# Kernel tuning notes

Hardware: AMD Instinct MI355X
Metric: run time of the kernel (lower is better)

Reference implementation:

```python
import jax, jax.numpy as jnp
import numpy as np

G, S, P = 128, 32, 16          # graphs, subgraphs per graph, nodes per subgraph
D, C, NH, OUT = 768, 256, 4, 7 # input dim, hidden dim, GAT heads, classes


def setup_inputs() -> dict:
    key = jax.random.key(0)
    ks = jax.random.split(key, 17)
    n = lambda k, shape, s=0.05: jax.random.normal(k, shape, dtype=jnp.float32) * s
    return {
        "x": jax.random.normal(ks[0], (G, S, P, D), dtype=jnp.float32),
        # GATConv(768 -> 256, heads=4, concat=False): lin weight, att vectors, bias
        "gat_W": n(ks[1], (D, NH * C)),
        "att_src": n(ks[2], (NH, C)),
        "att_dst": n(ks[3], (NH, C)),
        "gat_b": n(ks[4], (C,)),
        # GRU(256 -> 256), torch layout [3*H, in]
        "gru_Wih": n(ks[5], (3 * C, C)),
        "gru_Whh": n(ks[6], (3 * C, C)),
        "gru_bih": n(ks[7], (3 * C,)),
        "gru_bhh": n(ks[8], (3 * C,)),
        # scale_up_projection Linear(256 -> 768)
        "up_W": n(ks[9], (D, C)),
        "up_b": n(ks[10], (D,)),
        # speaker_projection Linear(1536 -> 768) + ReLU
        "sp_W": n(ks[11], (D, 2 * D)),
        "sp_b": n(ks[12], (D,)),
        # GlobalAttention gate Linear(256 -> 1)
        "att_W": n(ks[13], (1, C)),
        "att_b": n(ks[14], (1,)),
        # classifier Linear(256 -> 7)
        "cls_W": n(ks[15], (OUT, C)),
        "cls_b": n(ks[16], (OUT,)),
    }


def _gat(x, W, a_src, a_dst, b):
    # PyG GATConv on a star graph (speaker = local node 0 -> all others) with
    # default add_self_loops=True, negative_slope=0.2, concat=False (mean over heads).
    # x: [G, P, D]
    h = jnp.einsum('gpd,dhc->gphc', x, W.reshape(D, NH, C))     # per-head transform
    es = jnp.sum(h * a_src, -1)                                 # [G, P, NH]
    ed = jnp.sum(h * a_dst, -1)
    lrelu = lambda v: jnp.where(v > 0, v, 0.2 * v)
    e_spk = lrelu(es[:, :1] + ed)   # edge speaker -> t
    e_slf = lrelu(es + ed)          # self loop t -> t
    w = jax.nn.softmax(jnp.stack([e_spk, e_slf], -1), axis=-1)  # [G, P, NH, 2]
    # for t == 0 both terms are h[:,0] and weights sum to 1, matching the
    # speaker node receiving only its self loop.
    out = w[..., 0:1] * h[:, :1] + w[..., 1:2] * h              # [G, P, NH, C]
    return out.mean(axis=2) + b


def _gru_cell(xin, h, Wih, Whh, bih, bhh):
    gi = xin @ Wih.T + bih
    gh = h @ Whh.T + bhh
    ir, iz, inn = jnp.split(gi, 3, -1)
    hr, hz, hn = jnp.split(gh, 3, -1)
    r = jax.nn.sigmoid(ir + hr)
    z = jax.nn.sigmoid(iz + hz)
    return (1 - z) * jnp.tanh(inn + r * hn) + z * h


def _forward(x, gat_W, att_src, att_dst, gat_b, gru_Wih, gru_Whh, gru_bih, gru_bhh,
             up_W, up_b, sp_W, sp_b, att_W, att_b, cls_W, cls_b):
    g, s, p, d = x.shape
    m0 = _gat(x[:, 0], gat_W, att_src, att_dst, gat_b)  # [G, P, C]
    h0 = jnp.zeros((g, p, C), x.dtype)

    def step(carry, _):
        h_run, m_prev = carry
        # running GRU hidden over memory prefix, then one zero-input step
        # (equivalent to rerunning the GRU over [m_0..m_{j-1}, 0])
        h_run = _gru_cell(m_prev, h_run, gru_Wih, gru_Whh, gru_bih, gru_bhh)
        h_nxt = _gru_cell(jnp.zeros_like(h_run), h_run, gru_Wih, gru_Whh, gru_bih, gru_bhh)
        pooled = h_nxt @ up_W.T + up_b                  # [G, P, D]
        # faithful to source: non_speaker_indices covers ALL nodes (torch.equal
        # shape-mismatch bug), and speaker_info is read AFTER the overwrite,
        # so the speaker concat is [pooled, pooled] and raw x[:, j>=1] is unused.
        spk = jnp.concatenate([pooled[:, 0], pooled[:, 0]], -1)  # [G, 2D]
        spk = jax.nn.relu(spk @ sp_W.T + sp_b)
        x_new = pooled.at[:, 0].set(spk)
        m = _gat(x_new, gat_W, att_src, att_dst, gat_b)
        return (h_run, m), m

    (_, _), ms = jax.lax.scan(step, (h0, m0), None, length=s - 1)
    mem = jnp.concatenate([m0[None], ms], axis=0)        # [S, G, P, C]
    # GlobalAttention pool over the P nodes of each subgraph memory state
    gate = jax.nn.softmax(jnp.squeeze(mem @ att_W.T + att_b, -1), axis=-1)  # [S, G, P]
    pooled = jnp.einsum('sgp,sgpc->sgc', gate, mem)
    logits = pooled @ cls_W.T + cls_b                    # [S, G, OUT]
    # torch stacks graph-major: [G*S, 1, OUT]
    return jnp.transpose(logits, (1, 0, 2)).reshape(g * s, 1, OUT)


def reference(x, gat_W, att_src, att_dst, gat_b, gru_Wih, gru_Whh, gru_bih, gru_bhh,
              up_W, up_b, sp_W, sp_b, att_W, att_b, cls_W, cls_b):
    return _forward(x, gat_W, att_src, att_dst, gat_b, gru_Wih, gru_Whh, gru_bih,
                    gru_bhh, up_W, up_b, sp_W, sp_b, att_W, att_b, cls_W, cls_b)
```

## Files before the change

### kernel.cpp

```cpp
#include <hip/hip_runtime.h>
#include <math.h>

#define NG 128
#define NS 32
#define NP 16
#define ND 768
#define NC 256
#define NHD 4
#define NOUT 7
#define NR 2048

typedef unsigned short ushortT;
typedef short bf16x8 __attribute__((ext_vector_type(8)));
typedef float f32x4 __attribute__((ext_vector_type(4)));

__device__ __forceinline__ ushortT f2b(float f) {
    union { float f; unsigned u; } v; v.f = f;
    unsigned r = (v.u + 0x7FFF + ((v.u >> 16) & 1)) >> 16;
    return (ushortT)r;
}
__device__ __forceinline__ float sigf(float v) { return 1.f / (1.f + expf(-v)); }

#define MFMA16(a, b, c) __builtin_amdgcn_mfma_f32_16x16x32_bf16((a), (b), (c), 0, 0, 0)

__global__ __launch_bounds__(256) void bgemm_kernel(
    const ushortT* __restrict__ A, const ushortT* __restrict__ Bt,
    const float* __restrict__ bias, float* __restrict__ outF,
    ushortT* __restrict__ outH, int N, int K, int act, int rowStride)
{
    __shared__ short As[64 * 40];
    __shared__ short Bs[64 * 40];
    const int tid = threadIdx.x;
    const int lane = tid & 63, wid = tid >> 6;
    const int quad = lane >> 4, l15 = lane & 15;
    const int row0 = blockIdx.y * 64, col0 = blockIdx.x * 64;
    const int mh = (wid & 1) * 32, nh = (wid >> 1) * 32;
    const int sr = tid >> 2, skq = (tid & 3) * 8;
    const ushortT* aptr = A + (size_t)(row0 + sr) * K;
    const ushortT* bptr = Bt + (size_t)(col0 + sr) * K;

    f32x4 acc[2][2];
    for (int i = 0; i < 2; ++i)
        for (int j = 0; j < 2; ++j) acc[i][j] = (f32x4){0.f, 0.f, 0.f, 0.f};

    for (int kk = 0; kk < K; kk += 32) {
        __syncthreads();
        *(uint4*)&As[sr * 40 + skq] = *(const uint4*)(aptr + kk + skq);
        *(uint4*)&Bs[sr * 40 + skq] = *(const uint4*)(bptr + kk + skq);
        __syncthreads();
        bf16x8 af0 = *(const bf16x8*)&As[(mh + l15) * 40 + quad * 8];
        bf16x8 af1 = *(const bf16x8*)&As[(mh + 16 + l15) * 40 + quad * 8];
        bf16x8 bf0 = *(const bf16x8*)&Bs[(nh + l15) * 40 + quad * 8];
        bf16x8 bf1 = *(const bf16x8*)&Bs[(nh + 16 + l15) * 40 + quad * 8];
        acc[0][0] = MFMA16(af0, bf0, acc[0][0]);
        acc[0][1] = MFMA16(af0, bf1, acc[0][1]);
        acc[1][0] = MFMA16(af1, bf0, acc[1][0]);
        acc[1][1] = MFMA16(af1, bf1, acc[1][1]);
    }
#pragma unroll
    for (int mt = 0; mt < 2; ++mt)
#pragma unroll
        for (int nt = 0; nt < 2; ++nt) {
            const int gc = col0 + nh + nt * 16 + l15;
            const float bv = bias ? bias[gc] : 0.f;
#pragma unroll
            for (int r = 0; r < 4; ++r) {
                const int gr = (row0 + mh + mt * 16 + quad * 4 + r) * rowStride;
                float v = acc[mt][nt][r] + bv;
                if (act) v = fmaxf(v, 0.f);
                if (outF) outF[(size_t)gr * N + gc] = v;
                if (outH) outH[(size_t)gr * N + gc] = f2b(v);
            }
        }
}

__global__ __launch_bounds__(256) void gru1_mfma_kernel(
    const ushortT* __restrict__ mB, const ushortT* __restrict__ hB,
    const ushortT* __restrict__ WihB, const ushortT* __restrict__ WhhB,
    const float* __restrict__ bih, const float* __restrict__ bhh,
    float* __restrict__ hF, ushortT* __restrict__ hBout)
{
    __shared__ short As[2 * 32 * 264];
    __shared__ short Bs[384 * 40];
    const int tid = threadIdx.x;
    const int lane = tid & 63, wid = tid >> 6;
    const int quad = lane >> 4, l15 = lane & 15;
    const int row0 = blockIdx.y * 32;
    const int n0 = blockIdx.x * 64;
    const int mt = wid & 1, nhh = (wid >> 1) * 32;

    for (int c = tid; c < 2048; c += 256) {
        const int mat = c >> 10, r2 = c & 1023, row = r2 >> 5, kc = (r2 & 31) * 8;
        const ushortT* src = (mat ? hB : mB) + (size_t)(row0 + row) * NC + kc;
        *(uint4*)&As[mat * 8448 + row * 264 + kc] = *(const uint4*)src;
    }
    f32x4 acc[2][3][2];
    for (int w = 0; w < 2; ++w)
        for (int g = 0; g < 3; ++g)
            for (int n = 0; n < 2; ++n) acc[w][g][n] = (f32x4){0.f, 0.f, 0.f, 0.f};

    for (int kk = 0; kk < 256; kk += 32) {
        __syncthreads();
        for (int c = tid; c < 1536; c += 256) {
            const int j = c >> 2, kq = (c & 3) * 8;
            const int w = j / 192, j2 = j - w * 192, gt = j2 >> 6, nloc = j2 & 63;
            const ushortT* src = (w ? WhhB : WihB) +
                (size_t)(gt * 256 + n0 + nloc) * NC + kk + kq;
            *(uint4*)&Bs[j * 40 + kq] = *(const uint4*)src;
        }
        __syncthreads();
        bf16x8 af0 = *(const bf16x8*)&As[(mt * 16 + l15) * 264 + kk + quad * 8];
        bf16x8 af1 = *(const bf16x8*)&As[8448 + (mt * 16 + l15) * 264 + kk + quad * 8];
#pragma unroll
        for (int gt = 0; gt < 3; ++gt)
#pragma unroll
            for (int nt = 0; nt < 2; ++nt) {
                const int jb = gt * 64 + nhh + nt * 16 + l15;
                bf16x8 b0 = *(const bf16x8*)&Bs[jb * 40 + quad * 8];
                bf16x8 b1 = *(const bf16x8*)&Bs[(192 + jb) * 40 + quad * 8];
                acc[0][gt][nt] = MFMA16(af0, b0, acc[0][gt][nt]);
                acc[1][gt][nt] = MFMA16(af1, b1, acc[1][gt][nt]);
            }
    }
#pragma unroll
    for (int nt = 0; nt < 2; ++nt) {
        const int c = n0 + nhh + nt * 16 + l15;
        const float br = bih[c], bz = bih[256 + c], bn = bih[512 + c];
        const float cr = bhh[c], cz = bhh[256 + c], cn = bhh[512 + c];
#pragma unroll
        for (int r = 0; r < 4; ++r) {
            const int grow = row0 + mt * 16 + quad * 4 + r;
            const size_t idx = (size_t)grow * NC + c;
            const float hold = hF[idx];
            const float rg = sigf(acc[0][0][nt][r] + br + acc[1][0][nt][r] + cr);
            const float zg = sigf(acc[0][1][nt][r] + bz + acc[1][1][nt][r] + cz);
            const float ng = tanhf(acc[0][2][nt][r] + bn + rg * (acc[1][2][nt][r] + cn));
            const float hn = (1.f - zg) * ng + zg * hold;
            hF[idx] = hn;
            hBout[idx] = f2b(hn);
        }
    }
}

__global__ __launch_bounds__(256) void gru2_mfma_kernel(
    const ushortT* __restrict__ hB, const ushortT* __restrict__ WhhB,
    const float* __restrict__ bih, const float* __restrict__ bhh,
    const float* __restrict__ hF, ushortT* __restrict__ hnB,
    ushortT* __restrict__ h0c)
{
    __shared__ short As[32 * 264];
    __shared__ short Bs[192 * 40];
    const int tid = threadIdx.x;
    const int lane = tid & 63, wid = tid >> 6;
    const int quad = lane >> 4, l15 = lane & 15;
    const int row0 = blockIdx.y * 32;
    const int n0 = blockIdx.x * 64;
    const int mt = wid & 1, nhh = (wid >> 1) * 32;

    for (int c = tid; c < 1024; c += 256) {
        const int row = c >> 5, kc = (c & 31) * 8;
        *(uint4*)&As[row * 264 + kc] =
            *(const uint4*)(hB + (size_t)(row0 + row) * NC + kc);
    }
    f32x4 acc[3][2];
    for (int g = 0; g < 3; ++g)
        for (int n = 0; n < 2; ++n) acc[g][n] = (f32x4){0.f, 0.f, 0.f, 0.f};

    for (int kk = 0; kk < 256; kk += 32) {
        __syncthreads();
        for (int c = tid; c < 768; c += 256) {
            const int j = c >> 2, kq = (c & 3) * 8;
            const int gt = j >> 6, nloc = j & 63;
            *(uint4*)&Bs[j * 40 + kq] =
                *(const uint4*)(WhhB + (size_t)(gt * 256 + n0 + nloc) * NC + kk + kq);
        }
        __syncthreads();
        bf16x8 af = *(const bf16x8*)&As[(mt * 16 + l15) * 264 + kk + quad * 8];
#pragma unroll
        for (int gt = 0; gt < 3; ++gt)
#pragma unroll
            for (int nt = 0; nt < 2; ++nt) {
                const int jb = gt * 64 + nhh + nt * 16 + l15;
                bf16x8 b = *(const bf16x8*)&Bs[jb * 40 + quad * 8];
                acc[gt][nt] = MFMA16(af, b, acc[gt][nt]);
            }
    }
#pragma unroll
    for (int nt = 0; nt < 2; ++nt) {
        const int c = n0 + nhh + nt * 16 + l15;
        const float br = bih[c], bz = bih[256 + c], bn = bih[512 + c];
        const float cr = bhh[c], cz = bhh[256 + c], cn = bhh[512 + c];
#pragma unroll
        for (int r = 0; r < 4; ++r) {
            const int grow = row0 + mt * 16 + quad * 4 + r;
            const size_t idx = (size_t)grow * NC + c;
            const float rg = sigf(br + acc[0][nt][r] + cr);
            const float zg = sigf(bz + acc[1][nt][r] + cz);
            const float ng = tanhf(bn + rg * (acc[2][nt][r] + cn));
            const float hv = (1.f - zg) * ng + zg * hF[idx];
            const ushortT hb = f2b(hv);
            hnB[idx] = hb;
            if ((grow & 15) == 0) h0c[(size_t)(grow >> 4) * NC + c] = hb;
        }
    }
}

__global__ __launch_bounds__(256) void fin_kernel(
    const float* __restrict__ hbuf, const float* __restrict__ att_src,
    const float* __restrict__ att_dst, const float* __restrict__ gat_b,
    const float* __restrict__ attW, const float* __restrict__ attb,
    const float* __restrict__ clsW, const float* __restrict__ clsb,
    ushortT* __restrict__ mB, float* __restrict__ outp, int s)
{
    const int g = blockIdx.x, tid = threadIdx.x;
    const int lane = tid & 63, wid = tid >> 6;
    __shared__ float es_s[16][4], ed_s[16][4];
    __shared__ float m_s[16][260];
    __shared__ float gate_s[16];
    __shared__ float pooled_s[256];
    const float* hb = hbuf + (size_t)g * NP * (NHD * NC);

    for (int pi = 0; pi < 4; ++pi) {
        const int p = wid * 4 + pi;
        const float* row = hb + p * (NHD * NC);
        float ss[4] = {0.f, 0.f, 0.f, 0.f}, sd[4] = {0.f, 0.f, 0.f, 0.f};
#pragma unroll
        for (int i = 0; i < 16; ++i) {
            const int col = lane + 64 * i;
            const float v = row[col];
            ss[i >> 2] += v * att_src[col];
            sd[i >> 2] += v * att_dst[col];
        }
        for (int off = 32; off; off >>= 1)
#pragma unroll
            for (int h = 0; h < 4; ++h) {
                ss[h] += __shfl_down(ss[h], off);
                sd[h] += __shfl_down(sd[h], off);
            }
        if (lane == 0)
#pragma unroll
            for (int h = 0; h < 4; ++h) { es_s[p][h] = ss[h]; ed_s[p][h] = sd[h]; }
    }
    __syncthreads();
    {
        const int p = tid >> 4, cb = (tid & 15) * 16;
        float accv[16];
#pragma unroll
        for (int cj = 0; cj < 16; ++cj) accv[cj] = 0.f;
#pragma unroll
        for (int h = 0; h < 4; ++h) {
            float e1 = es_s[0][h] + ed_s[p][h]; e1 = e1 > 0.f ? e1 : 0.2f * e1;
            float e2 = es_s[p][h] + ed_s[p][h]; e2 = e2 > 0.f ? e2 : 0.2f * e2;
            const float mx = fmaxf(e1, e2);
            float w0 = expf(e1 - mx), w1 = expf(e2 - mx);
            const float inv = 1.f / (w0 + w1);
            w0 *= inv; w1 *= inv;
            const float* r0 = hb + h * NC + cb;
            const float* rp = hb + p * (NHD * NC) + h * NC + cb;
#pragma unroll
            for (int cj = 0; cj < 16; ++cj) accv[cj] += w0 * r0[cj] + w1 * rp[cj];
        }
#pragma unroll
        for (int cj = 0; cj < 16; ++cj) {
            const float v = accv[cj] * 0.25f + gat_b[cb + cj];
            m_s[p][cb + cj] = v;
            mB[(size_t)(g * NP + p) * NC + cb + cj] = f2b(v);
        }
    }
    __syncthreads();
    for (int pi = 0; pi < 4; ++pi) {
        const int p = wid * 4 + pi;
        float sg = 0.f;
#pragma unroll
        for (int i = 0; i < 4; ++i) { const int c = lane + 64 * i; sg += m_s[p][c] * attW[c]; }
        for (int off = 32; off; off >>= 1) sg += __shfl_down(sg, off);
        if (lane == 0) gate_s[p] = sg + attb[0];
    }
    __syncthreads();
    float mx = -1e30f;
#pragma unroll
    for (int p = 0; p < 16; ++p) mx = fmaxf(mx, gate_s[p]);
    float ge[16], ssum = 0.f;
#pragma unroll
    for (int p = 0; p < 16; ++p) { ge[p] = expf(gate_s[p] - mx); ssum += ge[p]; }
    const float inv = 1.f / ssum;
    {
        float pc = 0.f;
#pragma unroll
        for (int p = 0; p < 16; ++p) pc += ge[p] * m_s[p][tid];
        pooled_s[tid] = pc * inv;
    }
    __syncthreads();
    const int o = tid >> 5, l32 = tid & 31;
    if (o < NOUT) {
        float a = 0.f;
#pragma unroll
        for (int i = 0; i < 8; ++i) {
            const int c = l32 + 32 * i;
            a += pooled_s[c] * clsW[o * NC + c];
        }
        for (int off = 16; off; off >>= 1) a += __shfl_down(a, off);
        if (l32 == 0) outp[((size_t)g * NS + s) * NOUT + o] = a + clsb[o];
    }
}

__global__ __launch_bounds__(256) void cast_kernel(const float* __restrict__ a,
                                                   ushortT* __restrict__ b, int n) {
    const int i = blockIdx.x * 256 + threadIdx.x;
    if (i < n) b[i] = f2b(a[i]);
}
__global__ __launch_bounds__(256) void gatT_kernel(const float* __restrict__ gW,
                                                   ushortT* __restrict__ gB) {
    const int idx = blockIdx.x * 256 + threadIdx.x;
    const int c = idx / ND, d = idx - c * ND;
    gB[idx] = f2b(gW[(size_t)d * (NHD * NC) + c]);
}
__global__ __launch_bounds__(256) void upwT_kernel(const float* __restrict__ upW,
                                                   ushortT* __restrict__ o) {
    const int idx = blockIdx.x * 256 + threadIdx.x;
    const int k = idx / ND, d = idx - k * ND;
    o[idx] = f2b(upW[(size_t)d * NC + k]);
}
__global__ __launch_bounds__(256) void bcomb_kernel(const float* __restrict__ gW,
                                                    const float* __restrict__ up_b,
                                                    float* __restrict__ bc) {
    const int c = blockIdx.x * 256 + threadIdx.x;
    if (c >= NHD * NC) return;
    float a = 0.f;
    for (int d = 0; d < ND; ++d) a += up_b[d] * gW[(size_t)d * (NHD * NC) + c];
    bc[c] = a;
}
__global__ __launch_bounds__(256) void spwc_kernel(const float* __restrict__ spW,
                                                   float* __restrict__ o) {
    const int idx = blockIdx.x * 256 + threadIdx.x;
    const int r = idx / ND, d = idx - r * ND;
    o[idx] = spW[(size_t)r * (2 * ND) + d] + spW[(size_t)r * (2 * ND) + ND + d];
}
__global__ __launch_bounds__(256) void wus_kernel(const float* __restrict__ spWc,
                                                  const float* __restrict__ upW,
                                                  ushortT* __restrict__ WusB) {
    const int c = threadIdx.x;
    const int o0 = blockIdx.x * 16;
    float acc[16];
#pragma unroll
    for (int i = 0; i < 16; ++i) acc[i] = 0.f;
    for (int d = 0; d < ND; ++d) {
        const float u = upW[(size_t)d * NC + c];
#pragma unroll
        for (int i = 0; i < 16; ++i) acc[i] += spWc[(size_t)(o0 + i) * ND + d] * u;
    }
#pragma unroll
    for (int i = 0; i < 16; ++i) WusB[(size_t)(o0 + i) * NC + c] = f2b(acc[i]);
}
__global__ __launch_bounds__(256) void bus_kernel(const float* __restrict__ spWc,
                                                  const float* __restrict__ up_b,
                                                  const float* __restrict__ sp_b,
                                                  float* __restrict__ bus) {
    const int o = blockIdx.x * 256 + threadIdx.x;
    if (o >= ND) return;
    float a = sp_b[o];
    const float* sr = spWc + (size_t)o * ND;
    for (int d = 0; d < ND; ++d) a += sr[d] * up_b[d];
    bus[o] = a;
}
__global__ __launch_bounds__(256) void x0_kernel(const float* __restrict__ x,
                                                 ushortT* __restrict__ xb) {
    const int idx = blockIdx.x * 256 + threadIdx.x;
    const int row = idx / ND, d = idx - row * ND;
    const int g = row >> 4, p = row & 15;
    xb[idx] = f2b(x[((size_t)g * (NS * NP) + p) * ND + d]);
}
__global__ __launch_bounds__(256) void zh_kernel(float* hF, ushortT* hB) {
    const int idx = blockIdx.x * 256 + threadIdx.x;
    hF[idx] = 0.f;
    hB[idx] = 0;
}

extern "C" void kernel_launch(void* const* d_in, const int* in_sizes, int n_in,
                              void* d_out, int out_size, void* d_ws, size_t ws_size,
                              hipStream_t stream) {
    (void)in_sizes; (void)n_in; (void)out_size; (void)ws_size;
    const float* x       = (const float*)d_in[0];
    const float* gat_W   = (const float*)d_in[1];
    const float* att_src = (const float*)d_in[2];
    const float* att_dst = (const float*)d_in[3];
    const float* gat_b   = (const float*)d_in[4];
    const float* gru_Wih = (const float*)d_in[5];
    const float* gru_Whh = (const float*)d_in[6];
    const float* gru_bih = (const float*)d_in[7];
    const float* gru_bhh = (const float*)d_in[8];
    const float* up_W    = (const float*)d_in[9];
    const float* up_b    = (const float*)d_in[10];
    const float* sp_W    = (const float*)d_in[11];
    const float* sp_b    = (const float*)d_in[12];
    const float* att_W   = (const float*)d_in[13];
    const float* att_b   = (const float*)d_in[14];
    const float* cls_W   = (const float*)d_in[15];
    const float* cls_b   = (const float*)d_in[16];
    float* outp = (float*)d_out;

    char* w = (char*)d_ws;
    ushortT* xb    = (ushortT*)w; w += (size_t)NR * ND * 2;
    ushortT* WihB  = (ushortT*)w; w += (size_t)(3 * NC) * NC * 2;
    ushortT* WhhB  = (ushortT*)w; w += (size_t)(3 * NC) * NC * 2;
    ushortT* gatB  = (ushortT*)w; w += (size_t)(NHD * NC) * ND * 2;
    ushortT* WusB  = (ushortT*)w; w += (size_t)ND * NC * 2;
    ushortT* upWT  = (ushortT*)w; w += (size_t)NC * ND * 2;
    ushortT* WcombB= (ushortT*)w; w += (size_t)(NHD * NC) * NC * 2;
    float*   bcomb = (float*)w;   w += (size_t)(NHD * NC) * 4;
    float*   spWc  = (float*)w;   w += (size_t)ND * ND * 4;
    float*   bus   = (float*)w;   w += (size_t)ND * 4;
    float*   hF    = (float*)w;   w += (size_t)NR * NC * 4;
    ushortT* hB    = (ushortT*)w; w += (size_t)NR * NC * 2;
    ushortT* hnB   = (ushortT*)w; w += (size_t)NR * NC * 2;
    ushortT* h0c   = (ushortT*)w; w += (size_t)NG * NC * 2;
    ushortT* spkB  = (ushortT*)w; w += (size_t)NG * ND * 2;
    float*   hbuf  = (float*)w;   w += (size_t)NR * (NHD * NC) * 4;
    ushortT* mB    = (ushortT*)w; w += (size_t)NR * NC * 2;

    cast_kernel<<<768, 256, 0, stream>>>(gru_Wih, WihB, 3 * NC * NC);
    cast_kernel<<<768, 256, 0, stream>>>(gru_Whh, WhhB, 3 * NC * NC);
    gatT_kernel<<<(NHD * NC * ND) / 256, 256, 0, stream>>>(gat_W, gatB);
    upwT_kernel<<<(NC * ND) / 256, 256, 0, stream>>>(up_W, upWT);
    bcomb_kernel<<<(NHD * NC) / 256, 256, 0, stream>>>(gat_W, up_b, bcomb);
    spwc_kernel<<<(ND * ND) / 256, 256, 0, stream>>>(sp_W, spWc);
    wus_kernel<<<ND / 16, 256, 0, stream>>>(spWc, up_W, WusB);
    bus_kernel<<<3, 256, 0, stream>>>(spWc, up_b, sp_b, bus);
    x0_kernel<<<(NR * ND) / 256, 256, 0, stream>>>(x, xb);
    zh_kernel<<<(NR * NC) / 256, 256, 0, stream>>>(hF, hB);
    bgemm_kernel<<<dim3(NC / 64, (NHD * NC) / 64), 256, 0, stream>>>(
        gatB, upWT, nullptr, nullptr, WcombB, NC, ND, 0, 1);

    bgemm_kernel<<<dim3((NHD * NC) / 64, NR / 64), 256, 0, stream>>>(
        xb, gatB, nullptr, hbuf, nullptr, NHD * NC, ND, 0, 1);
    fin_kernel<<<NG, 256, 0, stream>>>(hbuf, att_src, att_dst, gat_b,
                                       att_W, att_b, cls_W, cls_b, mB, outp, 0);

    for (int j = 1; j < NS; ++j) {
        gru1_mfma_kernel<<<dim3(NC / 64, NR / 32), 256, 0, stream>>>(
            mB, hB, WihB, WhhB, gru_bih, gru_bhh, hF, hB);
        gru2_mfma_kernel<<<dim3(NC / 64, NR / 32), 256, 0, stream>>>(
            hB, WhhB, gru_bih, gru_bhh, hF, hnB, h0c);
        bgemm_kernel<<<dim3(ND / 64, NG / 64), 256, 0, stream>>>(
            h0c, WusB, bus, nullptr, spkB, ND, NC, 1, 1);
        bgemm_kernel<<<dim3((NHD * NC) / 64, NR / 64), 256, 0, stream>>>(
            hnB, WcombB, bcomb, hbuf, nullptr, NHD * NC, NC, 0, 1);
        bgemm_kernel<<<dim3((NHD * NC) / 64, NG / 64), 256, 0, stream>>>(
            spkB, gatB, nullptr, hbuf, nullptr, NHD * NC, ND, 0, 16);
        fin_kernel<<<NG, 256, 0, stream>>>(hbuf, att_src, att_dst, gat_b,
                                           att_W, att_b, cls_W, cls_b, mB, outp, j);
    }
}
```

Before: 2.630 ms.

## Fuse GRU steps and speaker projection per graph; merge GAT GEMM launches

Replaces the per-step gru1, gru2 and speaker-projection GEMM launches with one kernel that runs one block of 512 threads per graph. The block keeps the hidden state in shared memory across both GRU applications and computes the speaker projection with a scalar dot product. It also merges the hnB×Wcomb GEMM and the speaker×gatW override GEMM into one launch, with the main tiles skipping speaker rows to avoid write conflicts. This cuts launches and inter-kernel round trips per step, but each of only 128 blocks streams the full GRU weight matrices three times, which lowers parallelism and raises L2 traffic.

```diff
diff --git a/kernel.cpp b/kernel.cpp
--- a/kernel.cpp
+++ b/kernel.cpp
@@ -19,23 +19,177 @@
     unsigned r = (v.u + 0x7FFF + ((v.u >> 16) & 1)) >> 16;
     return (ushortT)r;
 }
+__device__ __forceinline__ float b2f(ushortT u) {
+    union { unsigned u; float f; } v; v.u = ((unsigned)u) << 16; return v.f;
+}
 __device__ __forceinline__ float sigf(float v) { return 1.f / (1.f + expf(-v)); }
 
 #define MFMA16(a, b, c) __builtin_amdgcn_mfma_f32_16x16x32_bf16((a), (b), (c), 0, 0, 0)
 
-__global__ __launch_bounds__(256) void bgemm_kernel(
-    const ushortT* __restrict__ A, const ushortT* __restrict__ Bt,
-    const float* __restrict__ bias, float* __restrict__ outF,
-    ushortT* __restrict__ outH, int N, int K, int act, int rowStride)
+__global__ __launch_bounds__(512) void gru12spk_kernel(
+    const ushortT* __restrict__ mB, const ushortT* __restrict__ hB,
+    float* __restrict__ hF,
+    const ushortT* __restrict__ WihB, const ushortT* __restrict__ WhhB,
+    const ushortT* __restrict__ WusB,
+    const float* __restrict__ bih, const float* __restrict__ bhh,
+    const float* __restrict__ busv,
+    ushortT* __restrict__ hBout, ushortT* __restrict__ hnB,
+    ushortT* __restrict__ spkB)
+{
+    __shared__ short Am[16 * 264];
+    __shared__ short Ah[16 * 264];
+    __shared__ short Bs[768 * 40];
+    const int g = blockIdx.x, tid = threadIdx.x;
+    const int w = tid >> 6, lane = tid & 63;
+    const int quad = lane >> 4, l15 = lane & 15;
+    const int row0 = g * 16;
+
+    {
+        const int row = tid >> 5, kc = (tid & 31) * 8;
+        *(uint4*)&Am[row * 264 + kc] = *(const uint4*)(mB + (size_t)(row0 + row) * NC + kc);
+        *(uint4*)&Ah[row * 264 + kc] = *(const uint4*)(hB + (size_t)(row0 + row) * NC + kc);
+    }
+
+    f32x4 ai[3][2], ah[3][2];
+#pragma unroll
+    for (int gt = 0; gt < 3; ++gt)
+#pragma unroll
+        for (int nf = 0; nf < 2; ++nf) {
+            ai[gt][nf] = (f32x4){0.f, 0.f, 0.f, 0.f};
+            ah[gt][nf] = (f32x4){0.f, 0.f, 0.f, 0.f};
+        }
+
+    for (int kk = 0; kk < NC; kk += 32) {
+        __syncthreads();
+        for (int s = tid; s < 3072; s += 512) {
+            const int row = s >> 2, kq = (s & 3) * 8;
+            *(uint4*)&Bs[row * 40 + kq] = *(const uint4*)(WihB + (size_t)row * NC + kk + kq);
+        }
+        __syncthreads();
+        bf16x8 af = *(const bf16x8*)&Am[l15 * 264 + kk + quad * 8];
+#pragma unroll
+        for (int gt = 0; gt < 3; ++gt)
+#pragma unroll
+            for (int nf = 0; nf < 2; ++nf) {
+                bf16x8 bv = *(const bf16x8*)&Bs[(gt * 256 + w * 32 + nf * 16 + l15) * 40 + quad * 8];
+                ai[gt][nf] = MFMA16(af, bv, ai[gt][nf]);
+            }
+    }
+    for (int kk = 0; kk < NC; kk += 32) {
+        __syncthreads();
+        for (int s = tid; s < 3072; s += 512) {
+            const int row = s >> 2, kq = (s & 3) * 8;
+            *(uint4*)&Bs[row * 40 + kq] = *(const uint4*)(WhhB + (size_t)row * NC + kk + kq);
+        }
+        __syncthreads();
+        bf16x8 af = *(const bf16x8*)&Ah[l15 * 264 + kk + quad * 8];
+#pragma unroll
+        for (int gt = 0; gt < 3; ++gt)
+#pragma unroll
+            for (int nf = 0; nf < 2; ++nf) {
+                bf16x8 bv = *(const bf16x8*)&Bs[(gt * 256 + w * 32 + nf * 16 + l15) * 40 + quad * 8];
+                ah[gt][nf] = MFMA16(af, bv, ah[gt][nf]);
+            }
+    }
+    float hreg[2][4];
+#pragma unroll
+    for (int nf = 0; nf < 2; ++nf) {
+        const int c = w * 32 + nf * 16 + l15;
+        const float br = bih[c], bz = bih[256 + c], bn = bih[512 + c];
+        const float cr = bhh[c], cz = bhh[256 + c], cn = bhh[512 + c];
+#pragma unroll
+        for (int r = 0; r < 4; ++r) {
+            const int row = quad * 4 + r;
+            const size_t idx = (size_t)(row0 + row) * NC + c;
+            const float hold = hF[idx];
+            const float rg = sigf(ai[0][nf][r] + br + ah[0][nf][r] + cr);
+            const float zg = sigf(ai[1][nf][r] + bz + ah[1][nf][r] + cz);
+            const float ng = tanhf(ai[2][nf][r] + bn + rg * (ah[2][nf][r] + cn));
+            const float hn = (1.f - zg) * ng + zg * hold;
+            hreg[nf][r] = hn;
+            hF[idx] = hn;
+            hBout[idx] = f2b(hn);
+            Am[row * 264 + c] = (short)f2b(hn);
+        }
+    }
+    f32x4 a2[3][2];
+#pragma unroll
+    for (int gt = 0; gt < 3; ++gt)
+#pragma unroll
+        for (int nf = 0; nf < 2; ++nf) a2[gt][nf] = (f32x4){0.f, 0.f, 0.f, 0.f};
+    for (int kk = 0; kk < NC; kk += 32) {
+        __syncthreads();
+        for (int s = tid; s < 3072; s += 512) {
+            const int row = s >> 2, kq = (s & 3) * 8;
+            *(uint4*)&Bs[row * 40 + kq] = *(const uint4*)(WhhB + (size_t)row * NC + kk + kq);
+        }
+        __syncthreads();
+        bf16x8 af = *(const bf16x8*)&Am[l15 * 264 + kk + quad * 8];
+#pragma unroll
+        for (int gt = 0; gt < 3; ++gt)
+#pragma unroll
+            for (int nf = 0; nf < 2; ++nf) {
+                bf16x8 bv = *(const bf16x8*)&Bs[(gt * 256 + w * 32 + nf * 16 + l15) * 40 + quad * 8];
+                a2[gt][nf] = MFMA16(af, bv, a2[gt][nf]);
+            }
+    }
+#pragma unroll
+    for (int nf = 0; nf < 2; ++nf) {
+        const int c = w * 32 + nf * 16 + l15;
+        const float br = bih[c], bz = bih[256 + c], bn = bih[512 + c];
+        const float cr = bhh[c], cz = bhh[256 + c], cn = bhh[512 + c];
+#pragma unroll
+        for (int r = 0; r < 4; ++r) {
+            const int row = quad * 4 + r;
+            const size_t idx = (size_t)(row0 + row) * NC + c;
+            const float rg = sigf(br + a2[0][nf][r] + cr);
+            const float zg = sigf(bz + a2[1][nf][r] + cz);
+            const float ng = tanhf(bn + rg * (a2[2][nf][r] + cn));
+            const float hv = (1.f - zg) * ng + zg * hreg[nf][r];
+            const ushortT hb16 = f2b(hv);
+            hnB[idx] = hb16;
+            Ah[row * 264 + c] = (short)hb16;
+        }
+    }
+    __syncthreads();
+    for (int o = tid; o < ND; o += 512) {
+        float s = busv[o];
+        const ushortT* wr = WusB + (size_t)o * NC;
+#pragma unroll 8
+        for (int k8 = 0; k8 < 32; ++k8) {
+            bf16x8 hv8 = *(const bf16x8*)&Ah[k8 * 8];
+            bf16x8 wv8 = *(const bf16x8*)(wr + k8 * 8);
+#pragma unroll
+            for (int i = 0; i < 8; ++i) s += b2f((ushortT)hv8[i]) * b2f((ushortT)wv8[i]);
+        }
+        spkB[(size_t)g * ND + o] = f2b(fmaxf(s, 0.f));
+    }
+}
+
+__global__ __launch_bounds__(256) void gatovr_kernel(
+    const ushortT* __restrict__ hnB, const ushortT* __restrict__ spkB,
+    const ushortT* __restrict__ WcombB, const ushortT* __restrict__ gatB,
+    const float* __restrict__ bcomb, float* __restrict__ hbuf)
 {
     __shared__ short As[64 * 40];
     __shared__ short Bs[64 * 40];
-    const int tid = threadIdx.x;
+    const int b = blockIdx.x, tid = threadIdx.x;
     const int lane = tid & 63, wid = tid >> 6;
     const int quad = lane >> 4, l15 = lane & 15;
-    const int row0 = blockIdx.y * 64, col0 = blockIdx.x * 64;
     const int mh = (wid & 1) * 32, nh = (wid >> 1) * 32;
     const int sr = tid >> 2, skq = (tid & 3) * 8;
+
+    const bool ovr = (b >= 512);
+    int row0, col0, K;
+    const ushortT *A, *Bt;
+    if (!ovr) {
+        row0 = (b >> 4) * 64; col0 = (b & 15) * 64;
+        A = hnB; Bt = WcombB; K = NC;
+    } else {
+        const int t = b - 512;
+        row0 = (t & 1) * 64; col0 = (t >> 1) * 64;
+        A = spkB; Bt = gatB; K = ND;
+    }
     const ushortT* aptr = A + (size_t)(row0 + sr) * K;
     const ushortT* bptr = Bt + (size_t)(col0 + sr) * K;
 
@@ -62,147 +216,18 @@
 #pragma unroll
         for (int nt = 0; nt < 2; ++nt) {
             const int gc = col0 + nh + nt * 16 + l15;
-            const float bv = bias ? bias[gc] : 0.f;
+            const float bv = ovr ? 0.f : bcomb[gc];
 #pragma unroll
             for (int r = 0; r < 4; ++r) {
-                const int gr = (row0 + mh + mt * 16 + quad * 4 + r) * rowStride;
-                float v = acc[mt][nt][r] + bv;
-                if (act) v = fmaxf(v, 0.f);
-                if (outF) outF[(size_t)gr * N + gc] = v;
-                if (outH) outH[(size_t)gr * N + gc] = f2b(v);
+                const int gr = row0 + mh + mt * 16 + quad * 4 + r;
+                const float v = acc[mt][nt][r] + bv;
+                if (ovr) {
+                    hbuf[(size_t)(gr * 16) * (NHD * NC) + gc] = v;
+                } else if (gr & 15) {
+                    hbuf[(size_t)gr * (NHD * NC) + gc] = v;
+                }
             }
         }
-}
-
-__global__ __launch_bounds__(256) void gru1_mfma_kernel(
-    const ushortT* __restrict__ mB, const ushortT* __restrict__ hB,
-    const ushortT* __restrict__ WihB, const ushortT* __restrict__ WhhB,
-    const float* __restrict__ bih, const float* __restrict__ bhh,
-    float* __restrict__ hF, ushortT* __restrict__ hBout)
-{
-    __shared__ short As[2 * 32 * 264];
-    __shared__ short Bs[384 * 40];
-    const int tid = threadIdx.x;
-    const int lane = tid & 63, wid = tid >> 6;
-    const int quad = lane >> 4, l15 = lane & 15;
-    const int row0 = blockIdx.y * 32;
-    const int n0 = blockIdx.x * 64;
-    const int mt = wid & 1, nhh = (wid >> 1) * 32;
-
-    for (int c = tid; c < 2048; c += 256) {
-        const int mat = c >> 10, r2 = c & 1023, row = r2 >> 5, kc = (r2 & 31) * 8;
-        const ushortT* src = (mat ? hB : mB) + (size_t)(row0 + row) * NC + kc;
-        *(uint4*)&As[mat * 8448 + row * 264 + kc] = *(const uint4*)src;
-    }
-    f32x4 acc[2][3][2];
-    for (int w = 0; w < 2; ++w)
-        for (int g = 0; g < 3; ++g)
-            for (int n = 0; n < 2; ++n) acc[w][g][n] = (f32x4){0.f, 0.f, 0.f, 0.f};
-
-    for (int kk = 0; kk < 256; kk += 32) {
-        __syncthreads();
-        for (int c = tid; c < 1536; c += 256) {
-            const int j = c >> 2, kq = (c & 3) * 8;
-            const int w = j / 192, j2 = j - w * 192, gt = j2 >> 6, nloc = j2 & 63;
-            const ushortT* src = (w ? WhhB : WihB) +
-                (size_t)(gt * 256 + n0 + nloc) * NC + kk + kq;
-            *(uint4*)&Bs[j * 40 + kq] = *(const uint4*)src;
-        }
-        __syncthreads();
-        bf16x8 af0 = *(const bf16x8*)&As[(mt * 16 + l15) * 264 + kk + quad * 8];
-        bf16x8 af1 = *(const bf16x8*)&As[8448 + (mt * 16 + l15) * 264 + kk + quad * 8];
-#pragma unroll
-        for (int gt = 0; gt < 3; ++gt)
-#pragma unroll
-            for (int nt = 0; nt < 2; ++nt) {
-                const int jb = gt * 64 + nhh + nt * 16 + l15;
-                bf16x8 b0 = *(const bf16x8*)&Bs[jb * 40 + quad * 8];
-                bf16x8 b1 = *(const bf16x8*)&Bs[(192 + jb) * 40 + quad * 8];
-                acc[0][gt][nt] = MFMA16(af0, b0, acc[0][gt][nt]);
-                acc[1][gt][nt] = MFMA16(af1, b1, acc[1][gt][nt]);
-            }
-    }
-#pragma unroll
-    for (int nt = 0; nt < 2; ++nt) {
-        const int c = n0 + nhh + nt * 16 + l15;
-        const float br = bih[c], bz = bih[256 + c], bn = bih[512 + c];
-        const float cr = bhh[c], cz = bhh[256 + c], cn = bhh[512 + c];
-#pragma unroll
-        for (int r = 0; r < 4; ++r) {
-            const int grow = row0 + mt * 16 + quad * 4 + r;
-            const size_t idx = (size_t)grow * NC + c;
-            const float hold = hF[idx];
-            const float rg = sigf(acc[0][0][nt][r] + br + acc[1][0][nt][r] + cr);
-            const float zg = sigf(acc[0][1][nt][r] + bz + acc[1][1][nt][r] + cz);
-            const float ng = tanhf(acc[0][2][nt][r] + bn + rg * (acc[1][2][nt][r] + cn));
-            const float hn = (1.f - zg) * ng + zg * hold;
-            hF[idx] = hn;
-            hBout[idx] = f2b(hn);
-        }
-    }
-}
-
-__global__ __launch_bounds__(256) void gru2_mfma_kernel(
-    const ushortT* __restrict__ hB, const ushortT* __restrict__ WhhB,
-    const float* __restrict__ bih, const float* __restrict__ bhh,
-    const float* __restrict__ hF, ushortT* __restrict__ hnB,
-    ushortT* __restrict__ h0c)
-{
-    __shared__ short As[32 * 264];
-    __shared__ short Bs[192 * 40];
-    const int tid = threadIdx.x;
-    const int lane = tid & 63, wid = tid >> 6;
-    const int quad = lane >> 4, l15 = lane & 15;
-    const int row0 = blockIdx.y * 32;
-    const int n0 = blockIdx.x * 64;
-    const int mt = wid & 1, nhh = (wid >> 1) * 32;
-
-    for (int c = tid; c < 1024; c += 256) {
-        const int row = c >> 5, kc = (c & 31) * 8;
-        *(uint4*)&As[row * 264 + kc] =
-            *(const uint4*)(hB + (size_t)(row0 + row) * NC + kc);
-    }
-    f32x4 acc[3][2];
-    for (int g = 0; g < 3; ++g)
-        for (int n = 0; n < 2; ++n) acc[g][n] = (f32x4){0.f, 0.f, 0.f, 0.f};
-
-    for (int kk = 0; kk < 256; kk += 32) {
-        __syncthreads();
-        for (int c = tid; c < 768; c += 256) {
-            const int j = c >> 2, kq = (c & 3) * 8;
-            const int gt = j >> 6, nloc = j & 63;
-            *(uint4*)&Bs[j * 40 + kq] =
-                *(const uint4*)(WhhB + (size_t)(gt * 256 + n0 + nloc) * NC + kk + kq);
-        }
-        __syncthreads();
-        bf16x8 af = *(const bf16x8*)&As[(mt * 16 + l15) * 264 + kk + quad * 8];
-#pragma unroll
-        for (int gt = 0; gt < 3; ++gt)
-#pragma unroll
-            for (int nt = 0; nt < 2; ++nt) {
-                const int jb = gt * 64 + nhh + nt * 16 + l15;
-                bf16x8 b = *(const bf16x8*)&Bs[jb * 40 + quad * 8];
-                acc[gt][nt] = MFMA16(af, b, acc[gt][nt]);
-            }
-    }
-#pragma unroll
-    for (int nt = 0; nt < 2; ++nt) {
-        const int c = n0 + nhh + nt * 16 + l15;
-        const float br = bih[c], bz = bih[256 + c], bn = bih[512 + c];
-        const float cr = bhh[c], cz = bhh[256 + c], cn = bhh[512 + c];
-#pragma unroll
-        for (int r = 0; r < 4; ++r) {
-            const int grow = row0 + mt * 16 + quad * 4 + r;
-            const size_t idx = (size_t)grow * NC + c;
-            const float rg = sigf(br + acc[0][nt][r] + cr);
-            const float zg = sigf(bz + acc[1][nt][r] + cz);
-            const float ng = tanhf(bn + rg * (acc[2][nt][r] + cn));
-            const float hv = (1.f - zg) * ng + zg * hF[idx];
-            const ushortT hb = f2b(hv);
-            hnB[idx] = hb;
-            if ((grow & 15) == 0) h0c[(size_t)(grow >> 4) * NC + c] = hb;
-        }
-    }
 }
 
 __global__ __launch_bounds__(256) void fin_kernel(
@@ -302,6 +327,57 @@
         for (int off = 16; off; off >>= 1) a += __shfl_down(a, off);
         if (l32 == 0) outp[((size_t)g * NS + s) * NOUT + o] = a + clsb[o];
     }
+}
+
+__global__ __launch_bounds__(256) void bgemm_kernel(
+    const ushortT* __restrict__ A, const ushortT* __restrict__ Bt,
+    const float* __restrict__ bias, float* __restrict__ outF,
+    ushortT* __restrict__ outH, int N, int K, int act)
+{
+    __shared__ short As[64 * 40];
+    __shared__ short Bs[64 * 40];
+    const int tid = threadIdx.x;
+    const int lane = tid & 63, wid = tid >> 6;
+    const int quad = lane >> 4, l15 = lane & 15;
+    const int row0 = blockIdx.y * 64, col0 = blockIdx.x * 64;
+    const int mh = (wid & 1) * 32, nh = (wid >> 1) * 32;
+    const int sr = tid >> 2, skq = (tid & 3) * 8;
+    const ushortT* aptr = A + (size_t)(row0 + sr) * K;
+    const ushortT* bptr = Bt + (size_t)(col0 + sr) * K;
+
+    f32x4 acc[2][2];
+    for (int i = 0; i < 2; ++i)
+        for (int j = 0; j < 2; ++j) acc[i][j] = (f32x4){0.f, 0.f, 0.f, 0.f};
+
+    for (int kk = 0; kk < K; kk += 32) {
+        __syncthreads();
+        *(uint4*)&As[sr * 40 + skq] = *(const uint4*)(aptr + kk + skq);
+        *(uint4*)&Bs[sr * 40 + skq] = *(const uint4*)(bptr + kk + skq);
+        __syncthreads();
+        bf16x8 af0 = *(const bf16x8*)&As[(mh + l15) * 40 + quad * 8];
+        bf16x8 af1 = *(const bf16x8*)&As[(mh + 16 + l15) * 40 + quad * 8];
+        bf16x8 bf0 = *(const bf16x8*)&Bs[(nh + l15) * 40 + quad * 8];
+        bf16x8 bf1 = *(const bf16x8*)&Bs[(nh + 16 + l15) * 40 + quad * 8];
+        acc[0][0] = MFMA16(af0, bf0, acc[0][0]);
+        acc[0][1] = MFMA16(af0, bf1, acc[0][1]);
+        acc[1][0] = MFMA16(af1, bf0, acc[1][0]);
+        acc[1][1] = MFMA16(af1, bf1, acc[1][1]);
+    }
+#pragma unroll
+    for (int mt = 0; mt < 2; ++mt)
+#pragma unroll
+        for (int nt = 0; nt < 2; ++nt) {
+            const int gc = col0 + nh + nt * 16 + l15;
+            const float bv = bias ? bias[gc] : 0.f;
+#pragma unroll
+            for (int r = 0; r < 4; ++r) {
+                const int gr = row0 + mh + mt * 16 + quad * 4 + r;
+                float v = acc[mt][nt][r] + bv;
+                if (act) v = fmaxf(v, 0.f);
+                if (outF) outF[(size_t)gr * N + gc] = v;
+                if (outH) outH[(size_t)gr * N + gc] = f2b(v);
+            }
+        }
 }
 
 __global__ __launch_bounds__(256) void cast_kernel(const float* __restrict__ a,
@@ -404,16 +480,15 @@
     ushortT* WihB  = (ushortT*)w; w += (size_t)(3 * NC) * NC * 2;
     ushortT* WhhB  = (ushortT*)w; w += (size_t)(3 * NC) * NC * 2;
     ushortT* gatB  = (ushortT*)w; w += (size_t)(NHD * NC) * ND * 2;
-    ushortT* WusB  = (ushortT*)w; w += (size_t)ND * NC * 2;
     ushortT* upWT  = (ushortT*)w; w += (size_t)NC * ND * 2;
     ushortT* WcombB= (ushortT*)w; w += (size_t)(NHD * NC) * NC * 2;
+    ushortT* WusB  = (ushortT*)w; w += (size_t)ND * NC * 2;
     float*   bcomb = (float*)w;   w += (size_t)(NHD * NC) * 4;
     float*   spWc  = (float*)w;   w += (size_t)ND * ND * 4;
     float*   bus   = (float*)w;   w += (size_t)ND * 4;
     float*   hF    = (float*)w;   w += (size_t)NR * NC * 4;
     ushortT* hB    = (ushortT*)w; w += (size_t)NR * NC * 2;
     ushortT* hnB   = (ushortT*)w; w += (size_t)NR * NC * 2;
-    ushortT* h0c   = (ushortT*)w; w += (size_t)NG * NC * 2;
     ushortT* spkB  = (ushortT*)w; w += (size_t)NG * ND * 2;
     float*   hbuf  = (float*)w;   w += (size_t)NR * (NHD * NC) * 4;
     ushortT* mB    = (ushortT*)w; w += (size_t)NR * NC * 2;
@@ -429,24 +504,18 @@
     x0_kernel<<<(NR * ND) / 256, 256, 0, stream>>>(x, xb);
     zh_kernel<<<(NR * NC) / 256, 256, 0, stream>>>(hF, hB);
     bgemm_kernel<<<dim3(NC / 64, (NHD * NC) / 64), 256, 0, stream>>>(
-        gatB, upWT, nullptr, nullptr, WcombB, NC, ND, 0, 1);
+        gatB, upWT, nullptr, nullptr, WcombB, NC, ND, 0);
 
     bgemm_kernel<<<dim3((NHD * NC) / 64, NR / 64), 256, 0, stream>>>(
-        xb, gatB, nullptr, hbuf, nullptr, NHD * NC, ND, 0, 1);
+        xb, gatB, nullptr, hbuf, nullptr, NHD * NC, ND, 0);
     fin_kernel<<<NG, 256, 0, stream>>>(hbuf, att_src, att_dst, gat_b,
                                        att_W, att_b, cls_W, cls_b, mB, outp, 0);
 
     for (int j = 1; j < NS; ++j) {
-        gru1_mfma_kernel<<<dim3(NC / 64, NR / 32), 256, 0, stream>>>(
-            mB, hB, WihB, WhhB, gru_bih, gru_bhh, hF, hB);
-        gru2_mfma_kernel<<<dim3(NC / 64, NR / 32), 256, 0, stream>>>(
-            hB, WhhB, gru_bih, gru_bhh, hF, hnB, h0c);
-        bgemm_kernel<<<dim3(ND / 64, NG / 64), 256, 0, stream>>>(
-            h0c, WusB, bus, nullptr, spkB, ND, NC, 1, 1);
-        bgemm_kernel<<<dim3((NHD * NC) / 64, NR / 64), 256, 0, stream>>>(
-            hnB, WcombB, bcomb, hbuf, nullptr, NHD * NC, NC, 0, 1);
-        bgemm_kernel<<<dim3((NHD * NC) / 64, NG / 64), 256, 0, stream>>>(
-            spkB, gatB, nullptr, hbuf, nullptr, NHD * NC, ND, 0, 16);
+        gru12spk_kernel<<<NG, 512, 0, stream>>>(
+            mB, hB, hF, WihB, WhhB, WusB, gru_bih, gru_bhh, bus, hB, hnB, spkB);
+        gatovr_kernel<<<544, 256, 0, stream>>>(
+            hnB, spkB, WcombB, gatB, bcomb, hbuf);
         fin_kernel<<<NG, 256, 0, stream>>>(hbuf, att_src, att_dst, gat_b,
                                            att_W, att_b, cls_W, cls_b, mB, outp, j);
     }
```

Measured after the change: 2.958 ms. 1.12x slower.
